# Kernel tuning notes

Measured on AMD Instinct MI355X. Metric: run time of the kernel, lower is better.

Reference implementation:

```python
import jax, jax.numpy as jnp
import numpy as np

NUM_HEADS = 16  # init_kwargs num_heads


def setup_inputs() -> dict:
    key = jax.random.key(0)
    ks = jax.random.split(key, 3)
    B, S, D = 4, 2048, 1024
    scale = 1.0 / np.sqrt(D)
    return {
        "x": jax.random.normal(ks[0], (B, S, D), dtype=jnp.float32),
        "in_proj_w": jax.random.normal(ks[1], (3 * D, D), dtype=jnp.float32) * scale,
        "in_proj_b": jnp.zeros((3 * D,), dtype=jnp.float32),
        "out_w": jax.random.normal(ks[2], (D, D), dtype=jnp.float32) * scale,
        "out_b": jnp.zeros((D,), dtype=jnp.float32),
        "gamma": jnp.ones((D,), dtype=jnp.float32),
        "beta": jnp.zeros((D,), dtype=jnp.float32),
    }


def reference(x, in_proj_w, in_proj_b, out_w, out_b, gamma, beta):
    B, S, D = x.shape
    H = NUM_HEADS
    hd = D // H
    # packed qkv projection (torch Linear convention: y = x @ W.T + b)
    qkv = x @ in_proj_w.T + in_proj_b            # [B,S,3D]
    q, k, v = jnp.split(qkv, 3, axis=-1)
    q = q.reshape(B, S, H, hd).transpose(0, 2, 1, 3)  # [B,H,S,hd]
    k = k.reshape(B, S, H, hd).transpose(0, 2, 1, 3)
    v = v.reshape(B, S, H, hd).transpose(0, 2, 1, 3)

    scores = jnp.einsum("bhqd,bhkd->bhqk", q, k) / jnp.sqrt(jnp.asarray(hd, x.dtype))
    # additive causal mask: -inf above the diagonal
    causal = jnp.tril(jnp.ones((S, S), dtype=bool))
    scores = jnp.where(causal, scores, jnp.asarray(-jnp.inf, scores.dtype))
    attn = jax.nn.softmax(scores, axis=-1)       # [B,H,S,S]

    ctx = jnp.einsum("bhqk,bhkd->bhqd", attn, v)  # [B,H,S,hd]
    ctx = ctx.transpose(0, 2, 1, 3).reshape(B, S, D)
    attn_out = ctx @ out_w.T + out_b

    y = x + attn_out
    mu = jnp.mean(y, axis=-1, keepdims=True)
    var = jnp.mean(jnp.square(y - mu), axis=-1, keepdims=True)
    y = (y - mu) * jax.lax.rsqrt(var + 1e-5) * gamma + beta
    return y
```

## Files before the change

### kernel.cpp

```cpp
#include <hip/hip_runtime.h>
#include <stdint.h>

typedef unsigned short u16;
typedef __bf16 bf16x8 __attribute__((ext_vector_type(8)));
typedef float  f32x4  __attribute__((ext_vector_type(4)));
typedef int    i32x4  __attribute__((ext_vector_type(4)));

__device__ __forceinline__ u16 f2bf(float f){
  union{float f; uint32_t u;} v; v.f = f;
  uint32_t r = v.u + 0x7FFFu + ((v.u >> 16) & 1u);
  return (u16)(r >> 16);
}

#define GLDS16(gp, lp) __builtin_amdgcn_global_load_lds( \
    (const __attribute__((address_space(1))) void*)(gp),  \
    (__attribute__((address_space(3))) void*)(lp), 16, 0, 0)

__global__ __launch_bounds__(256) void cvt_kernel(const float* __restrict__ in,
                                                  u16* __restrict__ out, int n4) {
  int stride = gridDim.x * blockDim.x;
  for (int i = blockIdx.x * blockDim.x + threadIdx.x; i < n4; i += stride) {
    float4 v = ((const float4*)in)[i];
    u16 o0 = f2bf(v.x), o1 = f2bf(v.y), o2 = f2bf(v.z), o3 = f2bf(v.w);
    u16* p = out + (size_t)i * 4;
    uint32_t lo = (uint32_t)o0 | ((uint32_t)o1 << 16);
    uint32_t hi = (uint32_t)o2 | ((uint32_t)o3 << 16);
    ((uint2*)p)[0] = make_uint2(lo, hi);
  }
}

template <int MODE>
__global__ __launch_bounds__(256) void gemm_bt(
    const u16* __restrict__ A, const u16* __restrict__ B,
    const float* __restrict__ bias,
    u16* __restrict__ Cbf, float* __restrict__ Cf, const float* __restrict__ resid,
    int M, int N, int K) {
  __shared__ u16 Alds[128 * 32];
  __shared__ u16 Blds[128 * 32];
  const int t = threadIdx.x;
  const int w = t >> 6, l = t & 63;
  const int wr = w >> 1, wc = w & 1;
  const int g = l >> 4, r16 = l & 15;

  const int gx = gridDim.x;
  const int nwg = gx * gridDim.y;
  const int wg = blockIdx.y * gx + blockIdx.x;
  const int cpx = nwg >> 3;
  const int swz = (wg & 7) * cpx + (wg >> 3);
  const int brow = (swz / gx) * 128, bcol = (swz % gx) * 128;

  f32x4 acc[4][4];
#pragma unroll
  for (int mi = 0; mi < 4; mi++)
#pragma unroll
    for (int nj = 0; nj < 4; nj++) acc[mi][nj] = (f32x4){0.f, 0.f, 0.f, 0.f};

  const int c0 = 2 * w, c1 = 2 * w + 1;
  const int srow0 = c0 * 16 + (l >> 2);
  const int srow1 = c1 * 16 + (l >> 2);
  const int scol = (l & 3) * 8;

  for (int kt = 0; kt < K; kt += 32) {
    __syncthreads();
    GLDS16(A + (size_t)(brow + srow0) * K + kt + scol, (char*)Alds + c0 * 1024);
    GLDS16(A + (size_t)(brow + srow1) * K + kt + scol, (char*)Alds + c1 * 1024);
    GLDS16(B + (size_t)(bcol + srow0) * K + kt + scol, (char*)Blds + c0 * 1024);
    GLDS16(B + (size_t)(bcol + srow1) * K + kt + scol, (char*)Blds + c1 * 1024);
    __syncthreads();

    bf16x8 af[4], bfr[4];
#pragma unroll
    for (int mi = 0; mi < 4; mi++)
      af[mi] = *(const bf16x8*)&Alds[(wr * 64 + mi * 16 + r16) * 32 + g * 8];
#pragma unroll
    for (int nj = 0; nj < 4; nj++)
      bfr[nj] = *(const bf16x8*)&Blds[(wc * 64 + nj * 16 + r16) * 32 + g * 8];
#pragma unroll
    for (int mi = 0; mi < 4; mi++)
#pragma unroll
      for (int nj = 0; nj < 4; nj++)
        acc[mi][nj] = __builtin_amdgcn_mfma_f32_16x16x32_bf16(af[mi], bfr[nj], acc[mi][nj], 0, 0, 0);
  }

#pragma unroll
  for (int mi = 0; mi < 4; mi++) {
#pragma unroll
    for (int nj = 0; nj < 4; nj++) {
      int col = bcol + wc * 64 + nj * 16 + r16;
      float bv = bias[col];
#pragma unroll
      for (int rr = 0; rr < 4; rr++) {
        int row = brow + wr * 64 + mi * 16 + g * 4 + rr;
        float v = acc[mi][nj][rr] + bv;
        if (MODE == 0) {
          Cbf[(size_t)row * N + col] = f2bf(v);
        } else {
          v += resid[(size_t)row * N + col];
          Cf[(size_t)row * N + col] = v;
        }
      }
    }
  }
}

__global__ __launch_bounds__(256) void vtrans_kernel(const u16* __restrict__ qkv,
                                                     u16* __restrict__ vtg) {
  const int S = 2048, HD3 = 3072;
  __shared__ u16 Vs[64 * 64];
  const int st = blockIdx.x, h = blockIdx.y, b = blockIdx.z;
  const int t = threadIdx.x;
  const int s0 = st * 64;
#pragma unroll
  for (int i = 0; i < 2; i++) {
    int n = t + i * 256;
    int row = n >> 3, c = n & 7;
    const u16* src = qkv + ((size_t)(b * S) + s0 + row) * HD3 + 2048 + h * 64 + c * 8;
    i32x4 v = *(const i32x4*)src;
    *(i32x4*)&Vs[row * 64 + ((c ^ (row & 7)) << 3)] = v;
  }
  __syncthreads();
  const int d = t >> 2;
  const int dc = d >> 3, dl = d & 7;
#pragma unroll
  for (int i = 0; i < 2; i++) {
    int kc = (t & 3) + i * 4;
    u16 tmp[8];
#pragma unroll
    for (int j = 0; j < 8; j++) {
      int k = kc * 8 + j;
      tmp[j] = Vs[k * 64 + ((dc ^ (k & 7)) << 3) + dl];
    }
    *(i32x4*)(vtg + ((size_t)(b * 16 + h) * 64 + d) * S + s0 + kc * 8) = *(i32x4*)tmp;
  }
}

__global__ __launch_bounds__(256) void attn_kernel(const u16* __restrict__ qkv,
                                                   const u16* __restrict__ vtg,
                                                   u16* __restrict__ ctxb) {
  const int S = 2048, HD3 = 3072;
  __shared__ u16 Kl[2][64 * 64];
  __shared__ u16 Vl[2][64 * 64];
  __shared__ u16 Pb[4][16 * 64];

  const int h = blockIdx.x & 15, b = blockIdx.x >> 4;
  const int pair = blockIdx.y;
  const int t = threadIdx.x, w = t >> 6, l = t & 63;
  const int g = l >> 4, r16 = l & 15;
  const size_t bS = (size_t)b * S;
  const size_t vbase = ((size_t)(b * 16 + h)) * 64 * S;

  const int srow = t >> 3, ssl = t & 7;
  const int scol = ((ssl ^ (srow & 7)) << 3);
  const int sdst = w * 1024;

  int kfo[4][2], pwo[4][2], pro[2];
#pragma unroll
  for (int f = 0; f < 4; f++) {
    int row = f * 16 + r16;
#pragma unroll
    for (int c = 0; c < 2; c++)
      kfo[f][c] = (row * 64 + (((c * 4 + g) ^ (row & 7)) << 3)) * 2;
#pragma unroll
    for (int q2 = 0; q2 < 2; q2++) {
      int kidx = f * 16 + g * 4 + q2 * 2;
      pwo[f][q2] = r16 * 128 + (((kidx >> 3) ^ (r16 & 7)) << 4) + ((kidx & 7) << 1);
    }
  }
#pragma unroll
  for (int kh = 0; kh < 2; kh++)
    pro[kh] = r16 * 128 + (((kh * 4 + g) ^ (r16 & 7)) << 4);

  const float QSC = 0.125f * 1.44269504f;

#define STAGE(bi_)                                                            \
  do {                                                                        \
    GLDS16(kp, (char*)Kl + (bi_)*8192 + sdst);                                \
    GLDS16(kp + 32 * HD3, (char*)Kl + (bi_)*8192 + 4096 + sdst);              \
    GLDS16(vp, (char*)Vl + (bi_)*8192 + sdst);                                \
    GLDS16(vp + 32 * S, (char*)Vl + (bi_)*8192 + 4096 + sdst);                \
    kp += 64 * HD3; vp += 64;                                                 \
  } while (0)

  for (int seg = 0; seg < 2; seg++) {
    const int qi = seg ? (15 - pair) : pair;
    const int q0w = qi * 128 + w * 32;
    const int nt = 2 * qi + 2;

    bf16x8 qf[2][2];
#pragma unroll
    for (int hh = 0; hh < 2; hh++) {
      const u16* qp = qkv + (bS + q0w + hh * 16 + r16) * HD3 + h * 64 + g * 8;
      bf16x8 a = *(const bf16x8*)qp;
      bf16x8 c = *(const bf16x8*)(qp + 32);
#pragma unroll
      for (int j = 0; j < 8; j++) {
        a[j] = (__bf16)((float)a[j] * QSC);
        c[j] = (__bf16)((float)c[j] * QSC);
      }
      qf[hh][0] = a; qf[hh][1] = c;
    }

    f32x4 ctx[2][4];
#pragma unroll
    for (int hh = 0; hh < 2; hh++)
#pragma unroll
      for (int f = 0; f < 4; f++) ctx[hh][f] = (f32x4){0.f, 0.f, 0.f, 0.f};
    float mrun[2] = {-1e30f, -1e30f};
    float lrun[2] = {0.f, 0.f};

    const u16* kp = qkv + (bS + srow) * HD3 + 1024 + h * 64 + scol;
    const u16* vp = vtg + vbase + (size_t)srow * S + scol;

    __syncthreads();
    STAGE(0);
    int cur = 0;
    for (int kt = 0; kt < nt; kt++) {
      const int k0 = kt * 64;
      asm volatile("s_waitcnt vmcnt(0)" ::: "memory");
      __syncthreads();
      if (kt + 1 < nt) STAGE(cur ^ 1);

      const char* KB = (const char*)Kl + cur * 8192;
      const char* VB = (const char*)Vl + cur * 8192;
      bf16x8 kf[4][2];
#pragma unroll
      for (int f = 0; f < 4; f++)
#pragma unroll
        for (int c = 0; c < 2; c++) kf[f][c] = *(const bf16x8*)(KB + kfo[f][c]);

#pragma unroll
      for (int hh = 0; hh < 2; hh++) {
        const int qmin = q0w + hh * 16;
        if (k0 >= qmin + 16) continue;

        f32x4 sf[4];
#pragma unroll
        for (int f = 0; f < 4; f++) {
          f32x4 s = (f32x4){0.f, 0.f, 0.f, 0.f};
          s = __builtin_amdgcn_mfma_f32_16x16x32_bf16(kf[f][0], qf[hh][0], s, 0, 0, 0);
          s = __builtin_amdgcn_mfma_f32_16x16x32_bf16(kf[f][1], qf[hh][1], s, 0, 0, 0);
          sf[f] = s;
        }
        const int qg = qmin + r16;
        if (k0 + 64 > qmin) {
#pragma unroll
          for (int f = 0; f < 4; f++)
#pragma unroll
            for (int rr = 0; rr < 4; rr++)
              if (k0 + f * 16 + g * 4 + rr > qg) sf[f][rr] = -1e30f;
        }

        float tm = sf[0][0];
#pragma unroll
        for (int f = 0; f < 4; f++)
#pragma unroll
          for (int rr = 0; rr < 4; rr++) tm = fmaxf(tm, sf[f][rr]);
        tm = fmaxf(tm, __shfl_xor(tm, 16, 64));
        tm = fmaxf(tm, __shfl_xor(tm, 32, 64));

        const float mold = mrun[hh];
        const bool skip = __all(tm <= mold + 8.0f);
        const float mnew = skip ? mold : fmaxf(mold, tm);
        mrun[hh] = mnew;

        float p[4][4];
        float ps = 0.f;
#pragma unroll
        for (int f = 0; f < 4; f++)
#pragma unroll
          for (int rr = 0; rr < 4; rr++) {
            p[f][rr] = exp2f(sf[f][rr] - mnew);
            ps += p[f][rr];
          }
        ps += __shfl_xor(ps, 16, 64);
        ps += __shfl_xor(ps, 32, 64);

        if (skip) {
          lrun[hh] += ps;
        } else {
          float sc = exp2f(mold - mnew);
          lrun[hh] = lrun[hh] * sc + ps;
#pragma unroll
          for (int rr = 0; rr < 4; rr++) {
            float scq = __shfl(sc, g * 4 + rr, 64);
#pragma unroll
            for (int f = 0; f < 4; f++) ctx[hh][f][rr] *= scq;
          }
        }

        char* PW = (char*)Pb + w * 2048;
#pragma unroll
        for (int f = 0; f < 4; f++)
#pragma unroll
          for (int q2 = 0; q2 < 2; q2++) {
            union { __bf16 b; u16 u; } a0, a1;
            a0.b = (__bf16)p[f][q2 * 2];
            a1.b = (__bf16)p[f][q2 * 2 + 1];
            *(uint32_t*)(PW + pwo[f][q2]) = (uint32_t)a0.u | ((uint32_t)a1.u << 16);
          }

        bf16x8 pf[2];
#pragma unroll
        for (int kh = 0; kh < 2; kh++) pf[kh] = *(const bf16x8*)(PW + pro[kh]);
#pragma unroll
        for (int f = 0; f < 4; f++)
#pragma unroll
          for (int kh = 0; kh < 2; kh++) {
            bf16x8 vf = *(const bf16x8*)(VB + kfo[f][kh]);
            ctx[hh][f] = __builtin_amdgcn_mfma_f32_16x16x32_bf16(pf[kh], vf, ctx[hh][f], 0, 0, 0);
          }
      }
      cur ^= 1;
    }

#pragma unroll
    for (int hh = 0; hh < 2; hh++) {
      float linv = 1.f / lrun[hh];
#pragma unroll
      for (int rr = 0; rr < 4; rr++) {
        float li = __shfl(linv, g * 4 + rr, 64);
        int qg = q0w + hh * 16 + g * 4 + rr;
#pragma unroll
        for (int f = 0; f < 4; f++) {
          union { __bf16 b; u16 u; } o;
          o.b = (__bf16)(ctx[hh][f][rr] * li);
          ctxb[(bS + qg) * 1024 + h * 64 + f * 16 + r16] = o.u;
        }
      }
    }
  }
#undef STAGE
}

__global__ __launch_bounds__(256) void ln_kernel(float* __restrict__ y,
                                                 const float* __restrict__ gamma,
                                                 const float* __restrict__ beta) {
  __shared__ float sh[4];
  const int row = blockIdx.x, t = threadIdx.x;
  const int w = t >> 6, l = t & 63;
  float4 v = ((const float4*)(y + (size_t)row * 1024))[t];
  float s = v.x + v.y + v.z + v.w;
#pragma unroll
  for (int m = 32; m; m >>= 1) s += __shfl_xor(s, m, 64);
  if (l == 0) sh[w] = s;
  __syncthreads();
  float mu = (sh[0] + sh[1] + sh[2] + sh[3]) * (1.0f / 1024.0f);
  float dx = v.x - mu, dy = v.y - mu, dz = v.z - mu, dw = v.w - mu;
  float ss = dx * dx + dy * dy + dz * dz + dw * dw;
#pragma unroll
  for (int m = 32; m; m >>= 1) ss += __shfl_xor(ss, m, 64);
  __syncthreads();
  if (l == 0) sh[w] = ss;
  __syncthreads();
  float var = (sh[0] + sh[1] + sh[2] + sh[3]) * (1.0f / 1024.0f);
  float rs = rsqrtf(var + 1e-5f);
  float4 gm = ((const float4*)gamma)[t];
  float4 bt = ((const float4*)beta)[t];
  float4 o;
  o.x = dx * rs * gm.x + bt.x;
  o.y = dy * rs * gm.y + bt.y;
  o.z = dz * rs * gm.z + bt.z;
  o.w = dw * rs * gm.w + bt.w;
  ((float4*)(y + (size_t)row * 1024))[t] = o;
}

extern "C" void kernel_launch(void* const* d_in, const int* in_sizes, int n_in,
                              void* d_out, int out_size, void* d_ws, size_t ws_size,
                              hipStream_t stream) {
  (void)in_sizes; (void)n_in; (void)out_size; (void)ws_size;
  const float* x     = (const float*)d_in[0];
  const float* w1    = (const float*)d_in[1];
  const float* b1    = (const float*)d_in[2];
  const float* w2    = (const float*)d_in[3];
  const float* b2    = (const float*)d_in[4];
  const float* gamma = (const float*)d_in[5];
  const float* beta  = (const float*)d_in[6];
  float* out = (float*)d_out;

  const int M = 8192, D = 1024, N1 = 3072;

  char* ws = (char*)d_ws;
  u16* x_bf   = (u16*)(ws);
  u16* w1_bf  = (u16*)(ws + 16777216);
  u16* w2_bf  = (u16*)(ws + 23068672);
  u16* qkv_bf = (u16*)(ws + 25165824);
  u16* ctx_bf = (u16*)(ws + 75497472);
  u16* vtg    = (u16*)(ws);

  cvt_kernel<<<2048, 256, 0, stream>>>(x, x_bf, M * D / 4);
  cvt_kernel<<<1024, 256, 0, stream>>>(w1, w1_bf, N1 * D / 4);
  cvt_kernel<<<512, 256, 0, stream>>>(w2, w2_bf, D * D / 4);

  gemm_bt<0><<<dim3(N1 / 128, M / 128), 256, 0, stream>>>(
      x_bf, w1_bf, b1, qkv_bf, nullptr, nullptr, M, N1, D);

  vtrans_kernel<<<dim3(32, 16, 4), 256, 0, stream>>>(qkv_bf, vtg);

  attn_kernel<<<dim3(64, 8), 256, 0, stream>>>(qkv_bf, vtg, ctx_bf);

  gemm_bt<1><<<dim3(D / 128, M / 128), 256, 0, stream>>>(
      ctx_bf, w2_bf, b2, nullptr, out, x, M, D, D);

  ln_kernel<<<M, 256, 0, stream>>>(out, gamma, beta);
}
```

Measured before the change: 318.6 us.

## Split attention query tile across 8 waves and add MFMA priority hints

Raises the attention block from 4 to 8 waves, so each wave handles one 16-row query group instead of two, and halves the per-thread K/V staging loads. K fragments are now read from LDS inside the score loop rather than preloaded, and s_setprio brackets the MFMA sections. The intent is more waves per block to hide latency and lower register pressure per wave. In exchange, block-wide syncs involve more waves, and waves whose causal range ends early sit idle at barriers.

```diff
diff --git a/kernel.cpp b/kernel.cpp
--- a/kernel.cpp
+++ b/kernel.cpp
@@ -134,13 +134,13 @@
   }
 }
 
-__global__ __launch_bounds__(256) void attn_kernel(const u16* __restrict__ qkv,
+__global__ __launch_bounds__(512) void attn_kernel(const u16* __restrict__ qkv,
                                                    const u16* __restrict__ vtg,
                                                    u16* __restrict__ ctxb) {
   const int S = 2048, HD3 = 3072;
   __shared__ u16 Kl[2][64 * 64];
   __shared__ u16 Vl[2][64 * 64];
-  __shared__ u16 Pb[4][16 * 64];
+  __shared__ u16 Pb[8][16 * 64];
 
   const int h = blockIdx.x & 15, b = blockIdx.x >> 4;
   const int pair = blockIdx.y;
@@ -171,42 +171,33 @@
     pro[kh] = r16 * 128 + (((kh * 4 + g) ^ (r16 & 7)) << 4);
 
   const float QSC = 0.125f * 1.44269504f;
+  char* PW = (char*)Pb + w * 2048;
 
 #define STAGE(bi_)                                                            \
   do {                                                                        \
     GLDS16(kp, (char*)Kl + (bi_)*8192 + sdst);                                \
-    GLDS16(kp + 32 * HD3, (char*)Kl + (bi_)*8192 + 4096 + sdst);              \
     GLDS16(vp, (char*)Vl + (bi_)*8192 + sdst);                                \
-    GLDS16(vp + 32 * S, (char*)Vl + (bi_)*8192 + 4096 + sdst);                \
     kp += 64 * HD3; vp += 64;                                                 \
   } while (0)
 
   for (int seg = 0; seg < 2; seg++) {
     const int qi = seg ? (15 - pair) : pair;
-    const int q0w = qi * 128 + w * 32;
+    const int qmin = qi * 128 + w * 16;
     const int nt = 2 * qi + 2;
 
-    bf16x8 qf[2][2];
-#pragma unroll
-    for (int hh = 0; hh < 2; hh++) {
-      const u16* qp = qkv + (bS + q0w + hh * 16 + r16) * HD3 + h * 64 + g * 8;
-      bf16x8 a = *(const bf16x8*)qp;
-      bf16x8 c = *(const bf16x8*)(qp + 32);
-#pragma unroll
-      for (int j = 0; j < 8; j++) {
-        a[j] = (__bf16)((float)a[j] * QSC);
-        c[j] = (__bf16)((float)c[j] * QSC);
-      }
-      qf[hh][0] = a; qf[hh][1] = c;
-    }
-
-    f32x4 ctx[2][4];
-#pragma unroll
-    for (int hh = 0; hh < 2; hh++)
-#pragma unroll
-      for (int f = 0; f < 4; f++) ctx[hh][f] = (f32x4){0.f, 0.f, 0.f, 0.f};
-    float mrun[2] = {-1e30f, -1e30f};
-    float lrun[2] = {0.f, 0.f};
+    const u16* qp = qkv + (bS + qmin + r16) * HD3 + h * 64 + g * 8;
+    bf16x8 qf0 = *(const bf16x8*)qp;
+    bf16x8 qf1 = *(const bf16x8*)(qp + 32);
+#pragma unroll
+    for (int j = 0; j < 8; j++) {
+      qf0[j] = (__bf16)((float)qf0[j] * QSC);
+      qf1[j] = (__bf16)((float)qf1[j] * QSC);
+    }
+
+    f32x4 ctx[4];
+#pragma unroll
+    for (int f = 0; f < 4; f++) ctx[f] = (f32x4){0.f, 0.f, 0.f, 0.f};
+    float mrun = -1e30f, lrun = 0.f;
 
     const u16* kp = qkv + (bS + srow) * HD3 + 1024 + h * 64 + scol;
     const u16* vp = vtg + vbase + (size_t)srow * S + scol;
@@ -220,27 +211,23 @@
       __syncthreads();
       if (kt + 1 < nt) STAGE(cur ^ 1);
 
-      const char* KB = (const char*)Kl + cur * 8192;
-      const char* VB = (const char*)Vl + cur * 8192;
-      bf16x8 kf[4][2];
-#pragma unroll
-      for (int f = 0; f < 4; f++)
-#pragma unroll
-        for (int c = 0; c < 2; c++) kf[f][c] = *(const bf16x8*)(KB + kfo[f][c]);
-
-#pragma unroll
-      for (int hh = 0; hh < 2; hh++) {
-        const int qmin = q0w + hh * 16;
-        if (k0 >= qmin + 16) continue;
+      if (k0 < qmin + 16) {
+        const char* KB = (const char*)Kl + cur * 8192;
+        const char* VB = (const char*)Vl + cur * 8192;
 
         f32x4 sf[4];
+        __builtin_amdgcn_s_setprio(1);
 #pragma unroll
         for (int f = 0; f < 4; f++) {
+          bf16x8 k0f = *(const bf16x8*)(KB + kfo[f][0]);
+          bf16x8 k1f = *(const bf16x8*)(KB + kfo[f][1]);
           f32x4 s = (f32x4){0.f, 0.f, 0.f, 0.f};
-          s = __builtin_amdgcn_mfma_f32_16x16x32_bf16(kf[f][0], qf[hh][0], s, 0, 0, 0);
-          s = __builtin_amdgcn_mfma_f32_16x16x32_bf16(kf[f][1], qf[hh][1], s, 0, 0, 0);
+          s = __builtin_amdgcn_mfma_f32_16x16x32_bf16(k0f, qf0, s, 0, 0, 0);
+          s = __builtin_amdgcn_mfma_f32_16x16x32_bf16(k1f, qf1, s, 0, 0, 0);
           sf[f] = s;
         }
+        __builtin_amdgcn_s_setprio(0);
+
         const int qg = qmin + r16;
         if (k0 + 64 > qmin) {
 #pragma unroll
@@ -258,10 +245,10 @@
         tm = fmaxf(tm, __shfl_xor(tm, 16, 64));
         tm = fmaxf(tm, __shfl_xor(tm, 32, 64));
 
-        const float mold = mrun[hh];
+        const float mold = mrun;
         const bool skip = __all(tm <= mold + 8.0f);
         const float mnew = skip ? mold : fmaxf(mold, tm);
-        mrun[hh] = mnew;
+        mrun = mnew;
 
         float p[4][4];
         float ps = 0.f;
@@ -276,19 +263,18 @@
         ps += __shfl_xor(ps, 32, 64);
 
         if (skip) {
-          lrun[hh] += ps;
+          lrun += ps;
         } else {
           float sc = exp2f(mold - mnew);
-          lrun[hh] = lrun[hh] * sc + ps;
+          lrun = lrun * sc + ps;
 #pragma unroll
           for (int rr = 0; rr < 4; rr++) {
             float scq = __shfl(sc, g * 4 + rr, 64);
 #pragma unroll
-            for (int f = 0; f < 4; f++) ctx[hh][f][rr] *= scq;
+            for (int f = 0; f < 4; f++) ctx[f][rr] *= scq;
           }
         }
 
-        char* PW = (char*)Pb + w * 2048;
 #pragma unroll
         for (int f = 0; f < 4; f++)
 #pragma unroll
@@ -302,30 +288,29 @@
         bf16x8 pf[2];
 #pragma unroll
         for (int kh = 0; kh < 2; kh++) pf[kh] = *(const bf16x8*)(PW + pro[kh]);
+        __builtin_amdgcn_s_setprio(1);
 #pragma unroll
         for (int f = 0; f < 4; f++)
 #pragma unroll
           for (int kh = 0; kh < 2; kh++) {
             bf16x8 vf = *(const bf16x8*)(VB + kfo[f][kh]);
-            ctx[hh][f] = __builtin_amdgcn_mfma_f32_16x16x32_bf16(pf[kh], vf, ctx[hh][f], 0, 0, 0);
+            ctx[f] = __builtin_amdgcn_mfma_f32_16x16x32_bf16(pf[kh], vf, ctx[f], 0, 0, 0);
           }
+        __builtin_amdgcn_s_setprio(0);
       }
       cur ^= 1;
     }
 
-#pragma unroll
-    for (int hh = 0; hh < 2; hh++) {
-      float linv = 1.f / lrun[hh];
-#pragma unroll
-      for (int rr = 0; rr < 4; rr++) {
-        float li = __shfl(linv, g * 4 + rr, 64);
-        int qg = q0w + hh * 16 + g * 4 + rr;
-#pragma unroll
-        for (int f = 0; f < 4; f++) {
-          union { __bf16 b; u16 u; } o;
-          o.b = (__bf16)(ctx[hh][f][rr] * li);
-          ctxb[(bS + qg) * 1024 + h * 64 + f * 16 + r16] = o.u;
-        }
+    float linv = 1.f / lrun;
+#pragma unroll
+    for (int rr = 0; rr < 4; rr++) {
+      float li = __shfl(linv, g * 4 + rr, 64);
+      int qg = qmin + g * 4 + rr;
+#pragma unroll
+      for (int f = 0; f < 4; f++) {
+        union { __bf16 b; u16 u; } o;
+        o.b = (__bf16)(ctx[f][rr] * li);
+        ctxb[(bS + qg) * 1024 + h * 64 + f * 16 + r16] = o.u;
       }
     }
   }
@@ -396,7 +381,7 @@
 
   vtrans_kernel<<<dim3(32, 16, 4), 256, 0, stream>>>(qkv_bf, vtg);
 
-  attn_kernel<<<dim3(64, 8), 256, 0, stream>>>(qkv_bf, vtg, ctx_bf);
+  attn_kernel<<<dim3(64, 8), 512, 0, stream>>>(qkv_bf, vtg, ctx_bf);
 
   gemm_bt<1><<<dim3(D / 128, M / 128), 256, 0, stream>>>(
       ctx_bf, w2_bf, b2, nullptr, out, x, M, D, D);
```

After: 305.1 us. 1.04x faster.
